# Optimization experiments

Measured on AMD Instinct MI355X. Metric: run time of the kernel, lower is better.

Reference implementation:

```python
import jax, jax.numpy as jnp
import numpy as np

N_NODES = 50000
N_FEAT = 128
N_RAND_EDGES = 800000
EPS = 1e-12


def _att_edge_weights(x, row, col, n_node):
    """GNNGuard att_coef: per-edge cosine sim, threshold, zero diagonal,
    row-wise L1 normalize, self-loop weight 1/(deg+1), then exp."""
    # cosine similarity per edge via normalized features (avoids NxN matrix)
    norms = jnp.sqrt(jnp.sum(x * x, axis=1, keepdims=True))
    xn = x / jnp.maximum(norms, EPS)
    sim = jnp.sum(xn[row] * xn[col], axis=1)          # [E]
    sim = jnp.where(sim < 0.1, 0.0, sim)              # threshold
    is_self = (row == col)
    sim = jnp.where(is_self, 0.0, sim)                # remove diagonal (self-sim==1)
    # row-wise L1 normalization (sim >= 0 after threshold)
    rowsum = jax.ops.segment_sum(sim, row, num_segments=n_node)
    rs = rowsum[row]
    sim_norm = jnp.where(rs > 0, sim / jnp.where(rs > 0, rs, 1.0), 0.0)
    # degree = number of nonzero normalized entries per row
    deg = jax.ops.segment_sum((sim_norm != 0).astype(sim.dtype), row,
                              num_segments=n_node)
    lam = 1.0 / (deg + 1.0)                           # self-loop gating weight
    w = jnp.where(is_self, lam[row], sim_norm)
    return jnp.exp(w)


def _gcn_conv(x, row, col, edge_weight, W, b, n_node):
    """GCNConv: h = XW; symmetric-normalized weighted aggregation + bias."""
    h = x @ W                                          # [N, out]
    deg = jax.ops.segment_sum(edge_weight, col, num_segments=n_node)
    dinv = jnp.where(deg > 0, jax.lax.rsqrt(jnp.where(deg > 0, deg, 1.0)), 0.0)
    norm = dinv[row] * edge_weight * dinv[col]         # [E]
    out = jax.ops.segment_sum(norm[:, None] * h[row], col, num_segments=n_node)
    return out + b


def setup_inputs() -> dict:
    key = jax.random.key(0)
    ks = jax.random.split(key, 10)
    x = jax.random.normal(ks[0], (N_NODES, N_FEAT), dtype=jnp.float32)
    # random edges with no self-loops, then append all self-loops
    row = jax.random.randint(ks[1], (N_RAND_EDGES,), 0, N_NODES, dtype=jnp.int32)
    off = jax.random.randint(ks[2], (N_RAND_EDGES,), 1, N_NODES, dtype=jnp.int32)
    col = (row + off) % N_NODES
    loops = jnp.arange(N_NODES, dtype=jnp.int32)
    edge_index = jnp.stack([jnp.concatenate([row, loops]),
                            jnp.concatenate([col, loops])], axis=0)
    s = 1.0 / np.sqrt(N_FEAT)
    W0 = jax.random.normal(ks[3], (N_FEAT, 128), dtype=jnp.float32) * s
    b0 = jnp.zeros((128,), dtype=jnp.float32)
    W1 = jax.random.normal(ks[4], (128, 128), dtype=jnp.float32) * s
    b1 = jnp.zeros((128,), dtype=jnp.float32)
    W2 = jax.random.normal(ks[5], (128, 40), dtype=jnp.float32) * s
    b2 = jnp.zeros((40,), dtype=jnp.float32)
    gate = jax.random.uniform(ks[6], (2,), dtype=jnp.float32)
    return {"x": x, "gate": gate, "W0": W0, "b0": b0, "W1": W1, "b1": b1,
            "W2": W2, "b2": b2, "edge_index": edge_index}


def reference(x, gate, W0, b0, W1, b1, W2, b2, edge_index):
    n = x.shape[0]
    row, col = edge_index[0], edge_index[1]
    Ws = [(W0, b0), (W1, b1), (W2, b2)]
    # layer 0: attention adj from raw features (kept as base adj for gating)
    adj_vals = _att_edge_weights(x, row, col, n)
    h = _gcn_conv(x, row, col, adj_vals, W0, b0, n)
    h = jax.nn.relu(h)
    for i in range(1, 3):
        e_new = _att_edge_weights(h, row, col, n)
        g = gate[i - 1]
        w = g * adj_vals + (1.0 - g) * e_new
        h = _gcn_conv(h, row, col, w, Ws[i][0], Ws[i][1], n)
        if i != 2:
            h = jax.nn.relu(h)
    return jax.nn.log_softmax(h, axis=1)
```

## Files before the change

kernel.cpp:

```cpp
#include <hip/hip_runtime.h>
#include <hip/hip_bf16.h>
#include <math.h>

#define F 128

typedef __attribute__((ext_vector_type(8))) short bf16x8;
typedef __attribute__((ext_vector_type(4))) float f32x4;

__global__ void k_normalize(const float* __restrict__ x, float* __restrict__ xn,
                            __hip_bfloat16* __restrict__ xnb, int N) {
  int wid = (blockIdx.x * blockDim.x + threadIdx.x) >> 6;
  int lane = threadIdx.x & 63;
  if (wid >= N) return;
  const float2* src = (const float2*)(x + (size_t)wid * F);
  float2 v = src[lane];
  float ss = v.x * v.x + v.y * v.y;
#pragma unroll
  for (int m = 32; m >= 1; m >>= 1) ss += __shfl_xor(ss, m);
  float inv = 1.0f / fmaxf(sqrtf(ss), 1e-12f);
  float2 o; o.x = v.x * inv; o.y = v.y * inv;
  ((float2*)(xn + (size_t)wid * F))[lane] = o;
  __hip_bfloat162 ob;
  ob.x = __float2bfloat16(o.x); ob.y = __float2bfloat16(o.y);
  ((__hip_bfloat162*)(xnb + (size_t)wid * F))[lane] = ob;
}


__global__ __launch_bounds__(256) void k_lhist(
    const int* __restrict__ keys, const int* __restrict__ perm,
    int* __restrict__ ghist, int* __restrict__ keyout, int nchunk, int E) {
  __shared__ int lh[256];
  int t = threadIdx.x, chunk = blockIdx.x;
  lh[t] = 0;
  __syncthreads();
  int base = chunk * 2048;
#pragma unroll
  for (int k = 0; k < 8; ++k) {
    int i = base + k * 256 + t;
    if (i < E) {
      int key = perm ? keys[perm[i]] : keys[i];
      if (keyout) keyout[i] = key;
      atomicAdd(&lh[key >> 8], 1);
    }
  }
  __syncthreads();
  ghist[t * nchunk + chunk] = lh[t];
}

__global__ void k_scan1(const int* __restrict__ cnt, int* __restrict__ partial,
                        int* __restrict__ bsum, int M) {
  __shared__ int sm[256];
  int t = threadIdx.x;
  int i = blockIdx.x * 256 + t;
  int val = (i < M) ? cnt[i] : 0;
  sm[t] = val;
  __syncthreads();
  for (int off = 1; off < 256; off <<= 1) {
    int v = (t >= off) ? sm[t - off] : 0;
    __syncthreads();
    sm[t] += v;
    __syncthreads();
  }
  if (i < M) partial[i] = sm[t] - val;
  if (t == 255) bsum[blockIdx.x] = sm[255];
}

__global__ void k_scan2(const int* __restrict__ bsum, int* __restrict__ boffs, int nb) {
  __shared__ int sm[256];
  int t = threadIdx.x;
  int carry = 0;
  for (int base = 0; base < nb; base += 256) {
    int idx = base + t;
    int val = (idx < nb) ? bsum[idx] : 0;
    sm[t] = val;
    __syncthreads();
    for (int off = 1; off < 256; off <<= 1) {
      int v = (t >= off) ? sm[t - off] : 0;
      __syncthreads();
      sm[t] += v;
      __syncthreads();
    }
    if (idx < nb) boffs[idx] = sm[t] - val + carry;
    carry += sm[255];
    __syncthreads();
  }
}

__global__ __launch_bounds__(256) void k_bucketize(
    const int* __restrict__ keys, const int* __restrict__ perm,
    const int* __restrict__ partial, const int* __restrict__ boffs,
    int* __restrict__ ebuck, int nchunk, int E) {
  __shared__ int lcur[256];
  int t = threadIdx.x, chunk = blockIdx.x;
  int idx = t * nchunk + chunk;
  lcur[t] = partial[idx] + boffs[idx >> 8];
  __syncthreads();
  int base = chunk * 2048;
#pragma unroll
  for (int k = 0; k < 8; ++k) {
    int i = base + k * 256 + t;
    if (i < E) {
      int key = perm ? keys[perm[i]] : keys[i];
      int pos = atomicAdd(&lcur[key >> 8], 1);
      ebuck[pos] = (i << 8) | (key & 255);
    }
  }
}

__global__ __launch_bounds__(256) void k_final_row(
    const int* __restrict__ ebuck, const int* __restrict__ partial,
    const int* __restrict__ boffs, int* __restrict__ perm_r,
    int* __restrict__ offs_r, int nchunk, int N, int E) {
  __shared__ int lh[256], sm[256], lscan[256];
  int t = threadIdx.x, b = blockIdx.x;
  int i0 = b * nchunk;
  int start = partial[i0] + boffs[i0 >> 8];
  int i1 = i0 + nchunk;
  int end = (b < 255) ? partial[i1] + boffs[i1 >> 8] : E;
  lh[t] = 0;
  __syncthreads();
  for (int p = start + t; p < end; p += 256) atomicAdd(&lh[ebuck[p] & 255], 1);
  __syncthreads();
  int val = lh[t];
  sm[t] = val;
  __syncthreads();
  for (int off = 1; off < 256; off <<= 1) {
    int v = (t >= off) ? sm[t - off] : 0;
    __syncthreads();
    sm[t] += v;
    __syncthreads();
  }
  lscan[t] = sm[t] - val;
  int node = b * 256 + t;
  if (node < N) offs_r[node] = start + lscan[t];
  if (b == 0 && t == 0) offs_r[N] = E;
  lh[t] = 0;
  __syncthreads();
  for (int p = start + t; p < end; p += 256) {
    int v = ebuck[p];
    int low = v & 255;
    int rk = atomicAdd(&lh[low], 1);
    perm_r[start + lscan[low] + rk] = v >> 8;
  }
}

__global__ __launch_bounds__(256) void k_final_col(
    const int* __restrict__ ebuck, const int* __restrict__ perm_r,
    const int* __restrict__ row, const int* __restrict__ partial,
    const int* __restrict__ boffs, int2* __restrict__ pstat,
    int* __restrict__ offs_c, int nchunk, int N, int E) {
  __shared__ int lh[256], sm[256], lscan[256];
  int t = threadIdx.x, b = blockIdx.x;
  int i0 = b * nchunk;
  int start = partial[i0] + boffs[i0 >> 8];
  int i1 = i0 + nchunk;
  int end = (b < 255) ? partial[i1] + boffs[i1 >> 8] : E;
  lh[t] = 0;
  __syncthreads();
  for (int p = start + t; p < end; p += 256) atomicAdd(&lh[ebuck[p] & 255], 1);
  __syncthreads();
  int val = lh[t];
  sm[t] = val;
  __syncthreads();
  for (int off = 1; off < 256; off <<= 1) {
    int v = (t >= off) ? sm[t - off] : 0;
    __syncthreads();
    sm[t] += v;
    __syncthreads();
  }
  lscan[t] = sm[t] - val;
  int node = b * 256 + t;
  if (node < N) offs_c[node] = start + lscan[t];
  if (b == 0 && t == 0) offs_c[N] = E;
  lh[t] = 0;
  __syncthreads();
  for (int p = start + t; p < end; p += 256) {
    int v = ebuck[p];
    int low = v & 255;
    int rp = v >> 8;
    int e = perm_r[rp];
    int rk = atomicAdd(&lh[low], 1);
    int2 rec; rec.x = row[e]; rec.y = rp;
    pstat[start + lscan[low] + rk] = rec;
  }
}

__global__ __launch_bounds__(256) void k_simw(
    const float* __restrict__ xn, const __hip_bfloat16* __restrict__ xnb,
    const int* __restrict__ colof_r, const int* __restrict__ offs_r,
    float* __restrict__ adjr, float* __restrict__ wgr,
    const float* __restrict__ gate, int layer, int N) {
  int w = threadIdx.x >> 6;
  int l = threadIdx.x & 63;
  int r = blockIdx.x * 4 + w;
  __shared__ float sims[4][320];
  __shared__ int scol[4][320];
  if (r >= N) return;
  int p0 = offs_r[r], p1 = offs_r[r + 1];
  int ne = p1 - p0;
  int quad = l >> 4;
  int m = l & 15;
  int qoff = quad * 8;
  const __hip_bfloat16* xr = xnb + (size_t)r * F;
  bf16x8 b0 = *(const bf16x8*)(xr + 0 * 32 + qoff);
  bf16x8 b1 = *(const bf16x8*)(xr + 1 * 32 + qoff);
  bf16x8 b2 = *(const bf16x8*)(xr + 2 * 32 + qoff);
  bf16x8 b3 = *(const bf16x8*)(xr + 3 * 32 + qoff);
  for (int tb = 0; tb < ne; tb += 16) {
    int ii = tb + m; if (ii > ne - 1) ii = ne - 1;
    int cm = colof_r[p0 + ii];
    if (quad == 0 && tb + m < ne) scol[w][tb + m] = cm;
    const __hip_bfloat16* xc = xnb + (size_t)cm * F;
    bf16x8 a0 = *(const bf16x8*)(xc + 0 * 32 + qoff);
    bf16x8 a1 = *(const bf16x8*)(xc + 1 * 32 + qoff);
    bf16x8 a2 = *(const bf16x8*)(xc + 2 * 32 + qoff);
    bf16x8 a3 = *(const bf16x8*)(xc + 3 * 32 + qoff);
    f32x4 acc = {0.f, 0.f, 0.f, 0.f};
    acc = __builtin_amdgcn_mfma_f32_16x16x32_bf16(a0, b0, acc, 0, 0, 0);
    acc = __builtin_amdgcn_mfma_f32_16x16x32_bf16(a1, b1, acc, 0, 0, 0);
    acc = __builtin_amdgcn_mfma_f32_16x16x32_bf16(a2, b2, acc, 0, 0, 0);
    acc = __builtin_amdgcn_mfma_f32_16x16x32_bf16(a3, b3, acc, 0, 0, 0);
    if (m == 0) {
#pragma unroll
      for (int reg = 0; reg < 4; ++reg) {
        int i = tb + quad * 4 + reg;
        if (i < ne) sims[w][i] = acc[reg];
      }
    }
  }
  float vsum = 0.f; int cn = 0;
  for (int base = 0; base < ne; base += 64) {
    int i = base + l;
    bool have = i < ne;
    float s = have ? sims[w][i] : 0.f;
    int c = have ? scol[w][i] : r;
    bool self = (c == r);
    bool flag = have && !self && fabsf(s - 0.1f) < 0.01f;
    unsigned long long mask = __ballot(flag);
    while (mask) {
      int src = __ffsll(mask) - 1;
      mask &= mask - 1;
      int cc = __shfl(c, src);
      float2 ar = ((const float2*)(xn + (size_t)r * F))[l];
      float2 bc = ((const float2*)(xn + (size_t)cc * F))[l];
      float d = ar.x * bc.x + ar.y * bc.y;
#pragma unroll
      for (int mm = 32; mm >= 1; mm >>= 1) d += __shfl_xor(d, mm);
      if (l == src) s = d;
    }
    if (self || s < 0.1f) s = 0.f;
    if (have) sims[w][i] = s;
    vsum += s;
    cn += (s > 0.f) ? 1 : 0;
  }
#pragma unroll
  for (int mm = 32; mm >= 1; mm >>= 1) {
    vsum += __shfl_xor(vsum, mm);
    cn += __shfl_xor(cn, mm);
  }
  float rs = vsum;
  float lam = 1.0f / (float)(cn + 1);
  float gg = (layer > 0) ? gate[layer - 1] : 0.f;
  for (int i = l; i < ne; i += 64) {
    int c = scol[w][i];
    float s = sims[w][i];
    float sn = (rs > 0.f) ? s / rs : 0.f;
    float wv = (c == r) ? lam : sn;
    wv = expf(wv);
    float wc;
    if (layer == 0) { adjr[p0 + i] = wv; wc = wv; }
    else { wc = gg * adjr[p0 + i] + (1.f - gg) * wv; }
    wgr[p0 + i] = wc;
  }
}

__global__ __launch_bounds__(256) void k_colw(
    const int2* __restrict__ pstat, const float* __restrict__ wgr,
    const int* __restrict__ offs_c, float* __restrict__ colw, int N) {
  int c = blockIdx.x * 256 + threadIdx.x;
  if (c >= N) return;
  int p0 = offs_c[c], p1 = offs_c[c + 1];
  float s = 0.f;
  int p = p0;
  for (; p + 4 <= p1; p += 4) {
    int2 a = pstat[p], b = pstat[p + 1], d = pstat[p + 2], e = pstat[p + 3];
    s += wgr[a.y] + wgr[b.y] + wgr[d.y] + wgr[e.y];
  }
  for (; p < p1; ++p) s += wgr[pstat[p].y];
  colw[c] = s;
}

__global__ __launch_bounds__(256) void k_gemm128(const float* __restrict__ A,
                                                 const float* __restrict__ W,
                                                 __hip_bfloat16* __restrict__ out, int M) {
  __shared__ float As[128][36];
  int t = threadIdx.x;
  int n0 = blockIdx.x * 32;
  for (int i = t; i < 32 * 128; i += 256) {
    int nn = i >> 7, kk = i & 127;
    int gn = n0 + nn;
    As[kk][nn] = (gn < M) ? A[(size_t)gn * 128 + kk] : 0.f;
  }
  __syncthreads();
  int nb = (t >> 6) * 8;
  int j2 = (t & 63) * 2;
  float acc[8][2] = {};
  for (int k = 0; k < 128; ++k) {
    float4 a01 = *(const float4*)&As[k][nb];
    float4 a23 = *(const float4*)&As[k][nb + 4];
    float2 wv = *(const float2*)&W[k * 128 + j2];
    acc[0][0] += a01.x * wv.x; acc[0][1] += a01.x * wv.y;
    acc[1][0] += a01.y * wv.x; acc[1][1] += a01.y * wv.y;
    acc[2][0] += a01.z * wv.x; acc[2][1] += a01.z * wv.y;
    acc[3][0] += a01.w * wv.x; acc[3][1] += a01.w * wv.y;
    acc[4][0] += a23.x * wv.x; acc[4][1] += a23.x * wv.y;
    acc[5][0] += a23.y * wv.x; acc[5][1] += a23.y * wv.y;
    acc[6][0] += a23.z * wv.x; acc[6][1] += a23.z * wv.y;
    acc[7][0] += a23.w * wv.x; acc[7][1] += a23.w * wv.y;
  }
  __hip_bfloat162* o2 = (__hip_bfloat162*)out;
#pragma unroll
  for (int i = 0; i < 8; ++i) {
    int gn = n0 + nb + i;
    if (gn < M) {
      __hip_bfloat162 o;
      o.x = __float2bfloat16(acc[i][0]); o.y = __float2bfloat16(acc[i][1]);
      o2[(size_t)gn * 64 + (j2 >> 1)] = o;
    }
  }
}

__global__ __launch_bounds__(320) void k_gemm40(const float* __restrict__ A,
                                                const float* __restrict__ W,
                                                __hip_bfloat16* __restrict__ out,
                                                int M, int C) {
  __shared__ float As[128][68];
  int t = threadIdx.x;
  int n0 = blockIdx.x * 64;
  for (int i = t; i < 64 * 128; i += 320) {
    int nn = i >> 7, kk = i & 127;
    int gn = n0 + nn;
    As[kk][nn] = (gn < M) ? A[(size_t)gn * 128 + kk] : 0.f;
  }
  __syncthreads();
  int gq = t / 40;
  int jc = t - gq * 40;
  int nb = gq * 8;
  float acc[8] = {};
  for (int k = 0; k < 128; ++k) {
    float4 a01 = *(const float4*)&As[k][nb];
    float4 a23 = *(const float4*)&As[k][nb + 4];
    float wv = W[k * C + jc];
    acc[0] += a01.x * wv; acc[1] += a01.y * wv; acc[2] += a01.z * wv; acc[3] += a01.w * wv;
    acc[4] += a23.x * wv; acc[5] += a23.y * wv; acc[6] += a23.z * wv; acc[7] += a23.w * wv;
  }
#pragma unroll
  for (int i = 0; i < 8; ++i) {
    int gn = n0 + nb + i;
    if (gn < M) out[(size_t)gn * C + jc] = __float2bfloat16(acc[i]);
  }
}

__global__ __launch_bounds__(256) void k_agg_norm(
    const __hip_bfloat162* __restrict__ hWb, const int2* __restrict__ pstat,
    const float* __restrict__ wgr, const float* __restrict__ colw,
    const int* __restrict__ offs_c, const float* __restrict__ bias,
    float* __restrict__ out, float* __restrict__ xn, __hip_bfloat16* __restrict__ xnb,
    int N) {
  int w = threadIdx.x >> 6;
  int t = threadIdx.x & 63;
  int c = blockIdx.x * 4 + w;
  if (c >= N) return;
  int p0 = offs_c[c], p1 = offs_c[c + 1];
  float dcv = colw[c];
  float dic = (dcv > 0.f) ? rsqrtf(dcv) : 0.f;
  float acc0 = bias[2 * t], acc1 = bias[2 * t + 1];
  int p = p0;
  for (; p + 8 <= p1; p += 8) {
    int2 s[8];
    __hip_bfloat162 h[8];
    float wv[8], dv[8];
#pragma unroll
    for (int k = 0; k < 8; ++k) s[k] = pstat[p + k];
#pragma unroll
    for (int k = 0; k < 8; ++k) h[k] = hWb[(size_t)s[k].x * 64 + t];
#pragma unroll
    for (int k = 0; k < 8; ++k) { wv[k] = wgr[s[k].y]; dv[k] = colw[s[k].x]; }
#pragma unroll
    for (int k = 0; k < 8; ++k) {
      float n = ((dv[k] > 0.f) ? rsqrtf(dv[k]) : 0.f) * wv[k] * dic;
      acc0 += n * __bfloat162float(h[k].x);
      acc1 += n * __bfloat162float(h[k].y);
    }
  }
  for (; p + 4 <= p1; p += 4) {
    int2 s0 = pstat[p], s1 = pstat[p + 1], s2 = pstat[p + 2], s3 = pstat[p + 3];
    float w0 = wgr[s0.y], w1 = wgr[s1.y], w2 = wgr[s2.y], w3 = wgr[s3.y];
    float d0 = colw[s0.x], d1 = colw[s1.x], d2 = colw[s2.x], d3 = colw[s3.x];
    __hip_bfloat162 h0 = hWb[(size_t)s0.x * 64 + t];
    __hip_bfloat162 h1 = hWb[(size_t)s1.x * 64 + t];
    __hip_bfloat162 h2 = hWb[(size_t)s2.x * 64 + t];
    __hip_bfloat162 h3 = hWb[(size_t)s3.x * 64 + t];
    float n0 = ((d0 > 0.f) ? rsqrtf(d0) : 0.f) * w0 * dic;
    float n1 = ((d1 > 0.f) ? rsqrtf(d1) : 0.f) * w1 * dic;
    float n2 = ((d2 > 0.f) ? rsqrtf(d2) : 0.f) * w2 * dic;
    float n3 = ((d3 > 0.f) ? rsqrtf(d3) : 0.f) * w3 * dic;
    acc0 += n0 * __bfloat162float(h0.x) + n1 * __bfloat162float(h1.x)
          + n2 * __bfloat162float(h2.x) + n3 * __bfloat162float(h3.x);
    acc1 += n0 * __bfloat162float(h0.y) + n1 * __bfloat162float(h1.y)
          + n2 * __bfloat162float(h2.y) + n3 * __bfloat162float(h3.y);
  }
  for (; p < p1; ++p) {
    int2 s0 = pstat[p];
    float w0 = wgr[s0.y];
    float d0 = colw[s0.x];
    __hip_bfloat162 h0 = hWb[(size_t)s0.x * 64 + t];
    float n0 = ((d0 > 0.f) ? rsqrtf(d0) : 0.f) * w0 * dic;
    acc0 += n0 * __bfloat162float(h0.x);
    acc1 += n0 * __bfloat162float(h0.y);
  }
  acc0 = fmaxf(acc0, 0.f); acc1 = fmaxf(acc1, 0.f);
  float2 o; o.x = acc0; o.y = acc1;
  ((float2*)out)[(size_t)c * 64 + t] = o;
  float ss = acc0 * acc0 + acc1 * acc1;
#pragma unroll
  for (int m = 32; m >= 1; m >>= 1) ss += __shfl_xor(ss, m);
  float inv = 1.0f / fmaxf(sqrtf(ss), 1e-12f);
  float2 on; on.x = acc0 * inv; on.y = acc1 * inv;
  ((float2*)xn)[(size_t)c * 64 + t] = on;
  __hip_bfloat162 ob;
  ob.x = __float2bfloat16(on.x); ob.y = __float2bfloat16(on.y);
  ((__hip_bfloat162*)xnb)[(size_t)c * 64 + t] = ob;
}

__global__ __launch_bounds__(256) void k_agg40_lsm(
    const __hip_bfloat16* __restrict__ hW, const int2* __restrict__ pstat,
    const float* __restrict__ wgr, const float* __restrict__ colw,
    const int* __restrict__ offs_c, const float* __restrict__ bias,
    float* __restrict__ out, int C, int N) {
  int w = threadIdx.x >> 6;
  int j = threadIdx.x & 63;
  int c = blockIdx.x * 4 + w;
  if (c >= N) return;
  int p0 = offs_c[c], p1 = offs_c[c + 1];
  float dcv = colw[c];
  float dic = (dcv > 0.f) ? rsqrtf(dcv) : 0.f;
  bool act = j < C;
  int jj = act ? j : 0;
  float acc = act ? bias[jj] : 0.f;
  int p = p0;
  for (; p + 4 <= p1; p += 4) {
    int2 s0 = pstat[p], s1 = pstat[p + 1], s2 = pstat[p + 2], s3 = pstat[p + 3];
    float w0 = wgr[s0.y], w1 = wgr[s1.y], w2 = wgr[s2.y], w3 = wgr[s3.y];
    float d0 = colw[s0.x], d1 = colw[s1.x], d2 = colw[s2.x], d3 = colw[s3.x];
    float h0 = __bfloat162float(hW[(size_t)s0.x * C + jj]);
    float h1 = __bfloat162float(hW[(size_t)s1.x * C + jj]);
    float h2 = __bfloat162float(hW[(size_t)s2.x * C + jj]);
    float h3 = __bfloat162float(hW[(size_t)s3.x * C + jj]);
    acc += ((d0 > 0.f) ? rsqrtf(d0) : 0.f) * w0 * dic * h0
         + ((d1 > 0.f) ? rsqrtf(d1) : 0.f) * w1 * dic * h1
         + ((d2 > 0.f) ? rsqrtf(d2) : 0.f) * w2 * dic * h2
         + ((d3 > 0.f) ? rsqrtf(d3) : 0.f) * w3 * dic * h3;
  }
  for (; p < p1; ++p) {
    int2 s0 = pstat[p];
    float w0 = wgr[s0.y];
    float d0 = colw[s0.x];
    acc += ((d0 > 0.f) ? rsqrtf(d0) : 0.f) * w0 * dic
         * __bfloat162float(hW[(size_t)s0.x * C + jj]);
  }
  if (!act) acc = 0.f;
  float v = act ? acc : -3.0e38f;
#pragma unroll
  for (int m = 32; m >= 1; m >>= 1) v = fmaxf(v, __shfl_xor(v, m));
  float ex = act ? expf(acc - v) : 0.f;
#pragma unroll
  for (int m = 32; m >= 1; m >>= 1) ex += __shfl_xor(ex, m);
  if (act) out[(size_t)c * C + j] = acc - v - logf(ex);
}

extern "C" void kernel_launch(void* const* d_in, const int* in_sizes, int n_in,
                              void* d_out, int out_size, void* d_ws, size_t ws_size,
                              hipStream_t stream) {
  const float* x    = (const float*)d_in[0];
  const float* gate = (const float*)d_in[1];
  const float* W0   = (const float*)d_in[2];
  const float* b0   = (const float*)d_in[3];
  const float* W1   = (const float*)d_in[4];
  const float* b1   = (const float*)d_in[5];
  const float* W2   = (const float*)d_in[6];
  const float* b2   = (const float*)d_in[7];
  const int* eidx   = (const int*)d_in[8];
  int N = in_sizes[0] / 128;
  int E = in_sizes[8] / 2;
  int C = in_sizes[7];
  const int* row = eidx;
  const int* col = eidx + E;

  char* ws = (char*)d_ws;
  size_t off = 0;
  auto alloc = [&](size_t bytes) {
    char* p = ws + off;
    off += (bytes + 255) & ~(size_t)255;
    return p;
  };
  float* xn     = (float*)alloc((size_t)N * 128 * 4);
  __hip_bfloat16* xnb = (__hip_bfloat16*)alloc((size_t)N * 128 * 2);
  float* bufC   = (float*)alloc((size_t)N * 128 * 4);
  __hip_bfloat16* hWb = (__hip_bfloat16*)alloc((size_t)N * 128 * 2);
  float* adjr   = (float*)alloc((size_t)E * 4);
  float* wgr    = (float*)alloc((size_t)E * 4);
  int*   perm_r = (int*)alloc((size_t)E * 4);
  int2*  pstat  = (int2*)alloc((size_t)E * 8);
  int*   colof_r= (int*)alloc((size_t)E * 4);
  int*   ebuck  = (int*)alloc((size_t)E * 4);
  int*   offs_c = (int*)alloc((size_t)(N + 1) * 4);
  int*   offs_r = (int*)alloc((size_t)(N + 1) * 4);
  float* colw   = (float*)alloc((size_t)N * 4);

  int NCHUNK = (E + 2047) / 2048;
  int M      = 256 * NCHUNK;
  int*   ghist  = (int*)alloc((size_t)M * 4);
  int*   partial= (int*)alloc((size_t)M * 4);
  int*   bsum   = (int*)alloc((size_t)NCHUNK * 4);
  int*   boffs  = (int*)alloc((size_t)NCHUNK * 4);

  int NBUK = (N + 255) / 256;
  int nb1  = (N + 255) / 256;
  int nw4  = (N + 3) / 4;

  k_lhist<<<NCHUNK, 256, 0, stream>>>(row, nullptr, ghist, nullptr, NCHUNK, E);
  k_scan1<<<NCHUNK, 256, 0, stream>>>(ghist, partial, bsum, M);
  k_scan2<<<1, 256, 0, stream>>>(bsum, boffs, NCHUNK);
  k_bucketize<<<NCHUNK, 256, 0, stream>>>(row, nullptr, partial, boffs, ebuck, NCHUNK, E);
  k_final_row<<<NBUK, 256, 0, stream>>>(ebuck, partial, boffs, perm_r, offs_r,
                                        NCHUNK, N, E);
  k_lhist<<<NCHUNK, 256, 0, stream>>>(col, perm_r, ghist, colof_r, NCHUNK, E);
  k_scan1<<<NCHUNK, 256, 0, stream>>>(ghist, partial, bsum, M);
  k_scan2<<<1, 256, 0, stream>>>(bsum, boffs, NCHUNK);
  k_bucketize<<<NCHUNK, 256, 0, stream>>>(col, perm_r, partial, boffs, ebuck, NCHUNK, E);
  k_final_col<<<NBUK, 256, 0, stream>>>(ebuck, perm_r, row, partial, boffs, pstat,
                                        offs_c, NCHUNK, N, E);

  for (int layer = 0; layer < 3; ++layer) {
    if (layer == 0) k_normalize<<<(N + 3) / 4, 256, 0, stream>>>(x, xn, xnb, N);
    k_simw<<<nw4, 256, 0, stream>>>(xn, xnb, colof_r, offs_r, adjr, wgr,
                                    gate, layer, N);
    k_colw<<<nb1, 256, 0, stream>>>(pstat, wgr, offs_c, colw, N);
    const float* hin = (layer == 0) ? x : bufC;
    if (layer < 2) {
      const float* W = (layer == 0) ? W0 : W1;
      const float* b = (layer == 0) ? b0 : b1;
      k_gemm128<<<(N + 31) / 32, 256, 0, stream>>>(hin, W, hWb, N);
      k_agg_norm<<<nw4, 256, 0, stream>>>((const __hip_bfloat162*)hWb, pstat, wgr, colw,
                                          offs_c, b, bufC, xn, xnb, N);
    } else {
      k_gemm40<<<(N + 63) / 64, 320, 0, stream>>>(hin, W2, hWb, N, C);
      k_agg40_lsm<<<nw4, 256, 0, stream>>>(hWb, pstat, wgr, colw, offs_c, b2,
                                           (float*)d_out, C, N);
    }
  }
}
```

Measured before the change: 592.5 us.

## Precompute per-edge GCN norm into packed records and store hidden state in bf16

A new kernel computes the full symmetric normalization dinv[row]*w*dinv[col] once per edge and packs it with the source index into an int2 record. The aggregation kernels then read one record per edge instead of doing the weight and degree gathers plus an rsqrt each time. The hidden activation buffer between layers moves from fp32 to bf16, which halves its write and read traffic in the GEMMs. The cost is one extra kernel launch and an extra E-sized pass per layer, plus some loss of precision in the layer input.

Measured after the change: 614.3 us. 1.04x slower.

```diff
diff --git a/kernel.cpp b/kernel.cpp
--- a/kernel.cpp
+++ b/kernel.cpp
@@ -24,7 +24,6 @@
   ob.x = __float2bfloat16(o.x); ob.y = __float2bfloat16(o.y);
   ((__hip_bfloat162*)(xnb + (size_t)wid * F))[lane] = ob;
 }
-
 
 __global__ __launch_bounds__(256) void k_lhist(
     const int* __restrict__ keys, const int* __restrict__ perm,
@@ -276,7 +275,7 @@
 
 __global__ __launch_bounds__(256) void k_colw(
     const int2* __restrict__ pstat, const float* __restrict__ wgr,
-    const int* __restrict__ offs_c, float* __restrict__ colw, int N) {
+    const int* __restrict__ offs_c, float* __restrict__ dinv, int N) {
   int c = blockIdx.x * 256 + threadIdx.x;
   if (c >= N) return;
   int p0 = offs_c[c], p1 = offs_c[c + 1];
@@ -287,10 +286,27 @@
     s += wgr[a.y] + wgr[b.y] + wgr[d.y] + wgr[e.y];
   }
   for (; p < p1; ++p) s += wgr[pstat[p].y];
-  colw[c] = s;
-}
-
-__global__ __launch_bounds__(256) void k_gemm128(const float* __restrict__ A,
+  dinv[c] = (s > 0.f) ? rsqrtf(s) : 0.f;
+}
+
+__global__ __launch_bounds__(256) void k_nrm(
+    const int2* __restrict__ pstat, const float* __restrict__ wgr,
+    const float* __restrict__ dinv, const int* __restrict__ offs_c,
+    int2* __restrict__ packed, int N) {
+  int c = blockIdx.x * 256 + threadIdx.x;
+  if (c >= N) return;
+  int p0 = offs_c[c], p1 = offs_c[c + 1];
+  float dic = dinv[c];
+  for (int p = p0; p < p1; ++p) {
+    int2 s = pstat[p];
+    float nrm = dinv[s.x] * wgr[s.y] * dic;
+    int2 rec; rec.x = s.x; rec.y = __float_as_int(nrm);
+    packed[p] = rec;
+  }
+}
+
+__global__ __launch_bounds__(256) void k_gemm128(const void* __restrict__ Av,
+                                                 int a_bf16,
                                                  const float* __restrict__ W,
                                                  __hip_bfloat16* __restrict__ out, int M) {
   __shared__ float As[128][36];
@@ -299,7 +315,12 @@
   for (int i = t; i < 32 * 128; i += 256) {
     int nn = i >> 7, kk = i & 127;
     int gn = n0 + nn;
-    As[kk][nn] = (gn < M) ? A[(size_t)gn * 128 + kk] : 0.f;
+    float v = 0.f;
+    if (gn < M) {
+      if (a_bf16) v = __bfloat162float(((const __hip_bfloat16*)Av)[(size_t)gn * 128 + kk]);
+      else v = ((const float*)Av)[(size_t)gn * 128 + kk];
+    }
+    As[kk][nn] = v;
   }
   __syncthreads();
   int nb = (t >> 6) * 8;
@@ -330,7 +351,7 @@
   }
 }
 
-__global__ __launch_bounds__(320) void k_gemm40(const float* __restrict__ A,
+__global__ __launch_bounds__(320) void k_gemm40(const __hip_bfloat16* __restrict__ A,
                                                 const float* __restrict__ W,
                                                 __hip_bfloat16* __restrict__ out,
                                                 int M, int C) {
@@ -340,7 +361,7 @@
   for (int i = t; i < 64 * 128; i += 320) {
     int nn = i >> 7, kk = i & 127;
     int gn = n0 + nn;
-    As[kk][nn] = (gn < M) ? A[(size_t)gn * 128 + kk] : 0.f;
+    As[kk][nn] = (gn < M) ? __bfloat162float(A[(size_t)gn * 128 + kk]) : 0.f;
   }
   __syncthreads();
   int gq = t / 40;
@@ -362,66 +383,55 @@
 }
 
 __global__ __launch_bounds__(256) void k_agg_norm(
-    const __hip_bfloat162* __restrict__ hWb, const int2* __restrict__ pstat,
-    const float* __restrict__ wgr, const float* __restrict__ colw,
+    const __hip_bfloat162* __restrict__ hWb, const int2* __restrict__ packed,
     const int* __restrict__ offs_c, const float* __restrict__ bias,
-    float* __restrict__ out, float* __restrict__ xn, __hip_bfloat16* __restrict__ xnb,
-    int N) {
+    __hip_bfloat16* __restrict__ outb, float* __restrict__ xn,
+    __hip_bfloat16* __restrict__ xnb, int N) {
   int w = threadIdx.x >> 6;
   int t = threadIdx.x & 63;
   int c = blockIdx.x * 4 + w;
   if (c >= N) return;
   int p0 = offs_c[c], p1 = offs_c[c + 1];
-  float dcv = colw[c];
-  float dic = (dcv > 0.f) ? rsqrtf(dcv) : 0.f;
   float acc0 = bias[2 * t], acc1 = bias[2 * t + 1];
   int p = p0;
   for (; p + 8 <= p1; p += 8) {
     int2 s[8];
     __hip_bfloat162 h[8];
-    float wv[8], dv[8];
-#pragma unroll
-    for (int k = 0; k < 8; ++k) s[k] = pstat[p + k];
+#pragma unroll
+    for (int k = 0; k < 8; ++k) s[k] = packed[p + k];
 #pragma unroll
     for (int k = 0; k < 8; ++k) h[k] = hWb[(size_t)s[k].x * 64 + t];
 #pragma unroll
-    for (int k = 0; k < 8; ++k) { wv[k] = wgr[s[k].y]; dv[k] = colw[s[k].x]; }
-#pragma unroll
     for (int k = 0; k < 8; ++k) {
-      float n = ((dv[k] > 0.f) ? rsqrtf(dv[k]) : 0.f) * wv[k] * dic;
+      float n = __int_as_float(s[k].y);
       acc0 += n * __bfloat162float(h[k].x);
       acc1 += n * __bfloat162float(h[k].y);
     }
   }
   for (; p + 4 <= p1; p += 4) {
-    int2 s0 = pstat[p], s1 = pstat[p + 1], s2 = pstat[p + 2], s3 = pstat[p + 3];
-    float w0 = wgr[s0.y], w1 = wgr[s1.y], w2 = wgr[s2.y], w3 = wgr[s3.y];
-    float d0 = colw[s0.x], d1 = colw[s1.x], d2 = colw[s2.x], d3 = colw[s3.x];
+    int2 s0 = packed[p], s1 = packed[p + 1], s2 = packed[p + 2], s3 = packed[p + 3];
     __hip_bfloat162 h0 = hWb[(size_t)s0.x * 64 + t];
     __hip_bfloat162 h1 = hWb[(size_t)s1.x * 64 + t];
     __hip_bfloat162 h2 = hWb[(size_t)s2.x * 64 + t];
     __hip_bfloat162 h3 = hWb[(size_t)s3.x * 64 + t];
-    float n0 = ((d0 > 0.f) ? rsqrtf(d0) : 0.f) * w0 * dic;
-    float n1 = ((d1 > 0.f) ? rsqrtf(d1) : 0.f) * w1 * dic;
-    float n2 = ((d2 > 0.f) ? rsqrtf(d2) : 0.f) * w2 * dic;
-    float n3 = ((d3 > 0.f) ? rsqrtf(d3) : 0.f) * w3 * dic;
+    float n0 = __int_as_float(s0.y), n1 = __int_as_float(s1.y);
+    float n2 = __int_as_float(s2.y), n3 = __int_as_float(s3.y);
     acc0 += n0 * __bfloat162float(h0.x) + n1 * __bfloat162float(h1.x)
           + n2 * __bfloat162float(h2.x) + n3 * __bfloat162float(h3.x);
     acc1 += n0 * __bfloat162float(h0.y) + n1 * __bfloat162float(h1.y)
           + n2 * __bfloat162float(h2.y) + n3 * __bfloat162float(h3.y);
   }
   for (; p < p1; ++p) {
-    int2 s0 = pstat[p];
-    float w0 = wgr[s0.y];
-    float d0 = colw[s0.x];
+    int2 s0 = packed[p];
     __hip_bfloat162 h0 = hWb[(size_t)s0.x * 64 + t];
-    float n0 = ((d0 > 0.f) ? rsqrtf(d0) : 0.f) * w0 * dic;
+    float n0 = __int_as_float(s0.y);
     acc0 += n0 * __bfloat162float(h0.x);
     acc1 += n0 * __bfloat162float(h0.y);
   }
   acc0 = fmaxf(acc0, 0.f); acc1 = fmaxf(acc1, 0.f);
-  float2 o; o.x = acc0; o.y = acc1;
-  ((float2*)out)[(size_t)c * 64 + t] = o;
+  __hip_bfloat162 oh;
+  oh.x = __float2bfloat16(acc0); oh.y = __float2bfloat16(acc1);
+  ((__hip_bfloat162*)outb)[(size_t)c * 64 + t] = oh;
   float ss = acc0 * acc0 + acc1 * acc1;
 #pragma unroll
   for (int m = 32; m >= 1; m >>= 1) ss += __shfl_xor(ss, m);
@@ -434,8 +444,7 @@
 }
 
 __global__ __launch_bounds__(256) void k_agg40_lsm(
-    const __hip_bfloat16* __restrict__ hW, const int2* __restrict__ pstat,
-    const float* __restrict__ wgr, const float* __restrict__ colw,
+    const __hip_bfloat16* __restrict__ hW, const int2* __restrict__ packed,
     const int* __restrict__ offs_c, const float* __restrict__ bias,
     float* __restrict__ out, int C, int N) {
   int w = threadIdx.x >> 6;
@@ -443,31 +452,22 @@
   int c = blockIdx.x * 4 + w;
   if (c >= N) return;
   int p0 = offs_c[c], p1 = offs_c[c + 1];
-  float dcv = colw[c];
-  float dic = (dcv > 0.f) ? rsqrtf(dcv) : 0.f;
   bool act = j < C;
   int jj = act ? j : 0;
   float acc = act ? bias[jj] : 0.f;
   int p = p0;
   for (; p + 4 <= p1; p += 4) {
-    int2 s0 = pstat[p], s1 = pstat[p + 1], s2 = pstat[p + 2], s3 = pstat[p + 3];
-    float w0 = wgr[s0.y], w1 = wgr[s1.y], w2 = wgr[s2.y], w3 = wgr[s3.y];
-    float d0 = colw[s0.x], d1 = colw[s1.x], d2 = colw[s2.x], d3 = colw[s3.x];
+    int2 s0 = packed[p], s1 = packed[p + 1], s2 = packed[p + 2], s3 = packed[p + 3];
     float h0 = __bfloat162float(hW[(size_t)s0.x * C + jj]);
     float h1 = __bfloat162float(hW[(size_t)s1.x * C + jj]);
     float h2 = __bfloat162float(hW[(size_t)s2.x * C + jj]);
     float h3 = __bfloat162float(hW[(size_t)s3.x * C + jj]);
-    acc += ((d0 > 0.f) ? rsqrtf(d0) : 0.f) * w0 * dic * h0
-         + ((d1 > 0.f) ? rsqrtf(d1) : 0.f) * w1 * dic * h1
-         + ((d2 > 0.f) ? rsqrtf(d2) : 0.f) * w2 * dic * h2
-         + ((d3 > 0.f) ? rsqrtf(d3) : 0.f) * w3 * dic * h3;
+    acc += __int_as_float(s0.y) * h0 + __int_as_float(s1.y) * h1
+         + __int_as_float(s2.y) * h2 + __int_as_float(s3.y) * h3;
   }
   for (; p < p1; ++p) {
-    int2 s0 = pstat[p];
-    float w0 = wgr[s0.y];
-    float d0 = colw[s0.x];
-    acc += ((d0 > 0.f) ? rsqrtf(d0) : 0.f) * w0 * dic
-         * __bfloat162float(hW[(size_t)s0.x * C + jj]);
+    int2 s0 = packed[p];
+    acc += __int_as_float(s0.y) * __bfloat162float(hW[(size_t)s0.x * C + jj]);
   }
   if (!act) acc = 0.f;
   float v = act ? acc : -3.0e38f;
@@ -505,18 +505,19 @@
     return p;
   };
   float* xn     = (float*)alloc((size_t)N * 128 * 4);
-  __hip_bfloat16* xnb = (__hip_bfloat16*)alloc((size_t)N * 128 * 2);
-  float* bufC   = (float*)alloc((size_t)N * 128 * 4);
-  __hip_bfloat16* hWb = (__hip_bfloat16*)alloc((size_t)N * 128 * 2);
+  __hip_bfloat16* xnb  = (__hip_bfloat16*)alloc((size_t)N * 128 * 2);
+  __hip_bfloat16* bufC = (__hip_bfloat16*)alloc((size_t)N * 128 * 2);
+  __hip_bfloat16* hWb  = (__hip_bfloat16*)alloc((size_t)N * 128 * 2);
   float* adjr   = (float*)alloc((size_t)E * 4);
   float* wgr    = (float*)alloc((size_t)E * 4);
   int*   perm_r = (int*)alloc((size_t)E * 4);
   int2*  pstat  = (int2*)alloc((size_t)E * 8);
+  int2*  packed = (int2*)alloc((size_t)E * 8);
   int*   colof_r= (int*)alloc((size_t)E * 4);
   int*   ebuck  = (int*)alloc((size_t)E * 4);
   int*   offs_c = (int*)alloc((size_t)(N + 1) * 4);
   int*   offs_r = (int*)alloc((size_t)(N + 1) * 4);
-  float* colw   = (float*)alloc((size_t)N * 4);
+  float* dinv   = (float*)alloc((size_t)N * 4);
 
   int NCHUNK = (E + 2047) / 2048;
   int M      = 256 * NCHUNK;
@@ -546,18 +547,20 @@
     if (layer == 0) k_normalize<<<(N + 3) / 4, 256, 0, stream>>>(x, xn, xnb, N);
     k_simw<<<nw4, 256, 0, stream>>>(xn, xnb, colof_r, offs_r, adjr, wgr,
                                     gate, layer, N);
-    k_colw<<<nb1, 256, 0, stream>>>(pstat, wgr, offs_c, colw, N);
-    const float* hin = (layer == 0) ? x : bufC;
+    k_colw<<<nb1, 256, 0, stream>>>(pstat, wgr, offs_c, dinv, N);
+    k_nrm<<<nb1, 256, 0, stream>>>(pstat, wgr, dinv, offs_c, packed, N);
     if (layer < 2) {
       const float* W = (layer == 0) ? W0 : W1;
       const float* b = (layer == 0) ? b0 : b1;
-      k_gemm128<<<(N + 31) / 32, 256, 0, stream>>>(hin, W, hWb, N);
-      k_agg_norm<<<nw4, 256, 0, stream>>>((const __hip_bfloat162*)hWb, pstat, wgr, colw,
-                                          offs_c, b, bufC, xn, xnb, N);
+      if (layer == 0)
+        k_gemm128<<<(N + 31) / 32, 256, 0, stream>>>((const void*)x, 0, W, hWb, N);
+      else
+        k_gemm128<<<(N + 31) / 32, 256, 0, stream>>>((const void*)bufC, 1, W, hWb, N);
+      k_agg_norm<<<nw4, 256, 0, stream>>>((const __hip_bfloat162*)hWb, packed, offs_c,
+                                          b, bufC, xn, xnb, N);
     } else {
-      k_gemm40<<<(N + 63) / 64, 320, 0, stream>>>(hin, W2, hWb, N, C);
-      k_agg40_lsm<<<nw4, 256, 0, stream>>>(hWb, pstat, wgr, colw, offs_c, b2,
-                                           (float*)d_out, C, N);
-    }
-  }
-}
+      k_gemm40<<<(N + 63) / 64, 320, 0, stream>>>(bufC, W2, hWb, N, C);
+      k_agg40_lsm<<<nw4, 256, 0, stream>>>(hWb, packed, offs_c, b2, (float*)d_out, C, N);
+    }
+  }
+}
```
